# Performance work log

Measured on AMD Instinct MI355X. Metric: run time of the kernel, lower is better.

Reference implementation:

```python
import jax, jax.numpy as jnp
from jax import lax
import numpy as np

B, S, D, STEPS = 16, 2048, 1024, 50

def setup_inputs() -> dict:
    key = jax.random.key(0)
    k1, k2, k3, k4 = jax.random.split(key, 4)
    latent = jax.random.normal(k1, (B, S, D), dtype=jnp.float32)
    W = jax.random.normal(k2, (D, 3), dtype=jnp.float32) * (1.0 / np.sqrt(D))
    b = jax.random.normal(k3, (3,), dtype=jnp.float32) * 0.02
    noise = jax.random.normal(k4, (B, S, 3), dtype=jnp.float32)
    return {"latent": latent, "W": W, "b": b, "noise": noise, "steps": STEPS}


def reference(latent, W, b, noise, steps):
    # target = coord_proj(latent)
    target = jnp.einsum("bsd,dc->bsc", latent, W) + b  # [B,S,3]
    # loop t = steps-1 .. 0, alpha = (t+1)/steps  ->  alphas = steps/steps, ..., 1/steps
    alphas = (jnp.arange(steps, 0, -1).astype(target.dtype)) / jnp.asarray(steps, target.dtype)
    def step(x, a):
        return a * x + (1.0 - a) * target, None
    x, _ = lax.scan(step, noise, alphas)
    return x
```

## Files before the change

### kernel.cpp

```cpp
#include <hip/hip_runtime.h>


#define D_DIM 1024
#define NCHUNK (D_DIM / 256)
#define RPW 4

__launch_bounds__(256, 3)
__global__ void diffusion_init_kernel(const float* __restrict__ latent,
                                      const float* __restrict__ W,
                                      const float* __restrict__ bias,
                                      const float* __restrict__ noise,
                                      const int* __restrict__ steps_p,
                                      float* __restrict__ out,
                                      int rows) {
    const int lane   = threadIdx.x & 63;
    const int wid    = (blockIdx.x * blockDim.x + threadIdx.x) >> 6;
    const int nwaves = (gridDim.x * blockDim.x) >> 6;

    float wv[NCHUNK][12];
    const float4* W4 = (const float4*)W;
    #pragma unroll
    for (int j = 0; j < NCHUNK; ++j) {
        #pragma unroll
        for (int q = 0; q < 3; ++q) {
            float4 t = W4[j * 192 + lane * 3 + q];
            wv[j][q * 4 + 0] = t.x;
            wv[j][q * 4 + 1] = t.y;
            wv[j][q * 4 + 2] = t.z;
            wv[j][q * 4 + 3] = t.w;
        }
    }
    const float b0 = bias[0], b1 = bias[1], b2 = bias[2];

    int steps = steps_p[0];
    if (steps <= 0 || steps > (1 << 20)) {
        float fs = __int_as_float(steps);
        steps = (fs >= 1.0f && fs < 1.0e6f) ? (int)(fs + 0.5f) : 50;
    }
    const int nt = steps < 2048 ? steps : 2048;
    float logp = 0.f;
    const float ls = __log2f((float)steps);
    for (int t = 1; t <= nt; ++t) logp += __log2f((float)t) - ls;
    const float P   = exp2f(logp);
    const float omP = 1.0f - P;

    const float4* L4 = (const float4*)latent;

    for (int base = wid * RPW; base < rows; base += nwaves * RPW) {
        float4 v[RPW][NCHUNK];
        #pragma unroll
        for (int r = 0; r < RPW; ++r) {
            const int row = base + r;
            if (row < rows) {
                const size_t rb = (size_t)row * (D_DIM / 4);
                #pragma unroll
                for (int j = 0; j < NCHUNK; ++j)
                    v[r][j] = L4[rb + j * 64 + lane];
            } else {
                #pragma unroll
                for (int j = 0; j < NCHUNK; ++j)
                    v[r][j] = make_float4(0.f, 0.f, 0.f, 0.f);
            }
        }

        float acc[RPW][3];
        #pragma unroll
        for (int r = 0; r < RPW; ++r) {
            float a0 = 0.f, a1 = 0.f, a2 = 0.f;
            #pragma unroll
            for (int j = 0; j < NCHUNK; ++j) {
                const float4 t = v[r][j];
                a0 = fmaf(t.x, wv[j][0], a0);
                a1 = fmaf(t.x, wv[j][1], a1);
                a2 = fmaf(t.x, wv[j][2], a2);
                a0 = fmaf(t.y, wv[j][3], a0);
                a1 = fmaf(t.y, wv[j][4], a1);
                a2 = fmaf(t.y, wv[j][5], a2);
                a0 = fmaf(t.z, wv[j][6], a0);
                a1 = fmaf(t.z, wv[j][7], a1);
                a2 = fmaf(t.z, wv[j][8], a2);
                a0 = fmaf(t.w, wv[j][9], a0);
                a1 = fmaf(t.w, wv[j][10], a1);
                a2 = fmaf(t.w, wv[j][11], a2);
            }
            acc[r][0] = a0; acc[r][1] = a1; acc[r][2] = a2;
        }

        #pragma unroll
        for (int off = 32; off > 0; off >>= 1) {
            #pragma unroll
            for (int r = 0; r < RPW; ++r) {
                acc[r][0] += __shfl_xor(acc[r][0], off, 64);
                acc[r][1] += __shfl_xor(acc[r][1], off, 64);
                acc[r][2] += __shfl_xor(acc[r][2], off, 64);
            }
        }

        if (lane < RPW) {
            const int row = base + lane;
            if (row < rows) {
                const float s0 = lane == 0 ? acc[0][0] : lane == 1 ? acc[1][0]
                               : lane == 2 ? acc[2][0] : acc[3][0];
                const float s1 = lane == 0 ? acc[0][1] : lane == 1 ? acc[1][1]
                               : lane == 2 ? acc[2][1] : acc[3][1];
                const float s2 = lane == 0 ? acc[0][2] : lane == 1 ? acc[1][2]
                               : lane == 2 ? acc[2][2] : acc[3][2];
                const size_t o = (size_t)row * 3;
                out[o + 0] = omP * (s0 + b0) + P * noise[o + 0];
                out[o + 1] = omP * (s1 + b1) + P * noise[o + 1];
                out[o + 2] = omP * (s2 + b2) + P * noise[o + 2];
            }
        }
    }
}

extern "C" void kernel_launch(void* const* d_in, const int* in_sizes, int n_in,
                              void* d_out, int out_size, void* d_ws, size_t ws_size,
                              hipStream_t stream) {
    const float* latent = (const float*)d_in[0];
    const float* W      = (const float*)d_in[1];
    const float* bias   = (const float*)d_in[2];
    const float* noise  = (const float*)d_in[3];
    const int*   steps  = (const int*)d_in[4];
    float* out = (float*)d_out;

    const int rows = in_sizes[3] / 3;

    const int blocks = (rows + (RPW * 4) - 1) / (RPW * 4);
    diffusion_init_kernel<<<blocks, 256, 0, stream>>>(latent, W, bias, noise,
                                                      steps, out, rows);
}
```

Measured before the change: 31.49 us.

## Switch to persistent grid with one-row software-pipelined nontemporal loads

After: 26.32 us. -16.4%, faster.

```diff
diff --git a/kernel.cpp b/kernel.cpp
--- a/kernel.cpp
+++ b/kernel.cpp
@@ -3,9 +3,10 @@
 
 #define D_DIM 1024
 #define NCHUNK (D_DIM / 256)
-#define RPW 4
 
-__launch_bounds__(256, 3)
+typedef float floatx4 __attribute__((ext_vector_type(4)));
+
+__launch_bounds__(256, 4)
 __global__ void diffusion_init_kernel(const float* __restrict__ latent,
                                       const float* __restrict__ W,
                                       const float* __restrict__ bias,
@@ -18,12 +19,12 @@
     const int nwaves = (gridDim.x * blockDim.x) >> 6;
 
     float wv[NCHUNK][12];
-    const float4* W4 = (const float4*)W;
+    const floatx4* W4 = (const floatx4*)W;
     #pragma unroll
     for (int j = 0; j < NCHUNK; ++j) {
         #pragma unroll
         for (int q = 0; q < 3; ++q) {
-            float4 t = W4[j * 192 + lane * 3 + q];
+            floatx4 t = W4[j * 192 + lane * 3 + q];
             wv[j][q * 4 + 0] = t.x;
             wv[j][q * 4 + 1] = t.y;
             wv[j][q * 4 + 2] = t.z;
@@ -44,73 +45,67 @@
     const float P   = exp2f(logp);
     const float omP = 1.0f - P;
 
-    const float4* L4 = (const float4*)latent;
+    const floatx4* L4 = (const floatx4*)latent;
 
-    for (int base = wid * RPW; base < rows; base += nwaves * RPW) {
-        float4 v[RPW][NCHUNK];
+    int row = wid;
+    floatx4 cur[NCHUNK];
+    if (row < rows) {
+        const size_t rb = (size_t)row * (D_DIM / 4);
         #pragma unroll
-        for (int r = 0; r < RPW; ++r) {
-            const int row = base + r;
-            if (row < rows) {
-                const size_t rb = (size_t)row * (D_DIM / 4);
-                #pragma unroll
-                for (int j = 0; j < NCHUNK; ++j)
-                    v[r][j] = L4[rb + j * 64 + lane];
-            } else {
-                #pragma unroll
-                for (int j = 0; j < NCHUNK; ++j)
-                    v[r][j] = make_float4(0.f, 0.f, 0.f, 0.f);
-            }
+        for (int j = 0; j < NCHUNK; ++j)
+            cur[j] = __builtin_nontemporal_load(&L4[rb + j * 64 + lane]);
+    }
+
+    for (; row < rows; row += nwaves) {
+        floatx4 nxt[NCHUNK];
+        const int nrow = row + nwaves;
+        if (nrow < rows) {
+            const size_t nb = (size_t)nrow * (D_DIM / 4);
+            #pragma unroll
+            for (int j = 0; j < NCHUNK; ++j)
+                nxt[j] = __builtin_nontemporal_load(&L4[nb + j * 64 + lane]);
+        } else {
+            #pragma unroll
+            for (int j = 0; j < NCHUNK; ++j) nxt[j] = (floatx4)(0.f);
         }
 
-        float acc[RPW][3];
+        float n0 = 0.f, n1 = 0.f, n2 = 0.f;
+        const size_t o = (size_t)row * 3;
+        if (lane == 0) { n0 = noise[o]; n1 = noise[o + 1]; n2 = noise[o + 2]; }
+
+        float a0 = 0.f, a1 = 0.f, a2 = 0.f;
         #pragma unroll
-        for (int r = 0; r < RPW; ++r) {
-            float a0 = 0.f, a1 = 0.f, a2 = 0.f;
-            #pragma unroll
-            for (int j = 0; j < NCHUNK; ++j) {
-                const float4 t = v[r][j];
-                a0 = fmaf(t.x, wv[j][0], a0);
-                a1 = fmaf(t.x, wv[j][1], a1);
-                a2 = fmaf(t.x, wv[j][2], a2);
-                a0 = fmaf(t.y, wv[j][3], a0);
-                a1 = fmaf(t.y, wv[j][4], a1);
-                a2 = fmaf(t.y, wv[j][5], a2);
-                a0 = fmaf(t.z, wv[j][6], a0);
-                a1 = fmaf(t.z, wv[j][7], a1);
-                a2 = fmaf(t.z, wv[j][8], a2);
-                a0 = fmaf(t.w, wv[j][9], a0);
-                a1 = fmaf(t.w, wv[j][10], a1);
-                a2 = fmaf(t.w, wv[j][11], a2);
-            }
-            acc[r][0] = a0; acc[r][1] = a1; acc[r][2] = a2;
+        for (int j = 0; j < NCHUNK; ++j) {
+            const floatx4 t = cur[j];
+            a0 = fmaf(t.x, wv[j][0], a0);
+            a1 = fmaf(t.x, wv[j][1], a1);
+            a2 = fmaf(t.x, wv[j][2], a2);
+            a0 = fmaf(t.y, wv[j][3], a0);
+            a1 = fmaf(t.y, wv[j][4], a1);
+            a2 = fmaf(t.y, wv[j][5], a2);
+            a0 = fmaf(t.z, wv[j][6], a0);
+            a1 = fmaf(t.z, wv[j][7], a1);
+            a2 = fmaf(t.z, wv[j][8], a2);
+            a0 = fmaf(t.w, wv[j][9], a0);
+            a1 = fmaf(t.w, wv[j][10], a1);
+            a2 = fmaf(t.w, wv[j][11], a2);
         }
 
         #pragma unroll
         for (int off = 32; off > 0; off >>= 1) {
-            #pragma unroll
-            for (int r = 0; r < RPW; ++r) {
-                acc[r][0] += __shfl_xor(acc[r][0], off, 64);
-                acc[r][1] += __shfl_xor(acc[r][1], off, 64);
-                acc[r][2] += __shfl_xor(acc[r][2], off, 64);
-            }
+            a0 += __shfl_xor(a0, off, 64);
+            a1 += __shfl_xor(a1, off, 64);
+            a2 += __shfl_xor(a2, off, 64);
         }
 
-        if (lane < RPW) {
-            const int row = base + lane;
-            if (row < rows) {
-                const float s0 = lane == 0 ? acc[0][0] : lane == 1 ? acc[1][0]
-                               : lane == 2 ? acc[2][0] : acc[3][0];
-                const float s1 = lane == 0 ? acc[0][1] : lane == 1 ? acc[1][1]
-                               : lane == 2 ? acc[2][1] : acc[3][1];
-                const float s2 = lane == 0 ? acc[0][2] : lane == 1 ? acc[1][2]
-                               : lane == 2 ? acc[2][2] : acc[3][2];
-                const size_t o = (size_t)row * 3;
-                out[o + 0] = omP * (s0 + b0) + P * noise[o + 0];
-                out[o + 1] = omP * (s1 + b1) + P * noise[o + 1];
-                out[o + 2] = omP * (s2 + b2) + P * noise[o + 2];
-            }
+        if (lane == 0) {
+            out[o + 0] = omP * (a0 + b0) + P * n0;
+            out[o + 1] = omP * (a1 + b1) + P * n1;
+            out[o + 2] = omP * (a2 + b2) + P * n2;
         }
+
+        #pragma unroll
+        for (int j = 0; j < NCHUNK; ++j) cur[j] = nxt[j];
     }
 }
 
@@ -126,7 +121,7 @@
 
     const int rows = in_sizes[3] / 3;
 
-    const int blocks = (rows + (RPW * 4) - 1) / (RPW * 4);
+    const int blocks = 1024;
     diffusion_init_kernel<<<blocks, 256, 0, stream>>>(latent, W, bias, noise,
                                                       steps, out, rows);
 }
```
